# Optimization experiments

Hardware: AMD Instinct MI355X
Metric: run time of the kernel (lower is better)

The kernel has to match this reference:

```python
import jax, jax.numpy as jnp
import numpy as np

B, LI, LJ, D = 32, 512, 512, 512
NN_DIM = 256  # agg output dim = 2*NN_DIM = 512


def setup_inputs() -> dict:
    key = jax.random.key(0)
    k1, k2, k3 = jax.random.split(key, 3)
    i = jax.random.normal(k1, (B, LI, D), dtype=jnp.float32)
    j = jax.random.normal(k2, (B, LJ, D), dtype=jnp.float32)
    W_agg = jax.random.normal(k3, (D, 2 * NN_DIM), dtype=jnp.float32) * (1.0 / np.sqrt(D))
    b_agg = jnp.zeros((2 * NN_DIM,), dtype=jnp.float32)
    return {"i": i, "j": j, "W_agg": W_agg, "b_agg": b_agg}


def _agg(x, W, b):
    # shared aggregation net: Dense(2*nn_dim) + tanh, then mean-pool over time
    # x: [B, L, D] -> [B, 2*nn_dim]
    return jnp.mean(jnp.tanh(jnp.einsum('bld,dh->blh', x, W) + b), axis=1)


def reference(i, j, W_agg, b_agg):
    # cross-attention scores: [B, Li, Lj]
    weight = jnp.einsum('bik,bjk->bij', i, j)
    # row softmax (over Lj) -> weights to aggregate j per i-position
    weight_j = jax.nn.softmax(weight, axis=2)
    # column softmax (over Li) -> weights to aggregate i per j-position
    weight_i = jax.nn.softmax(weight, axis=1)
    weighted_i = jnp.einsum('bij,bid->bjd', weight_i, i)  # [B, Lj, D]
    weighted_j = jnp.einsum('bij,bjd->bid', weight_j, j)  # [B, Li, D]
    output_i = jnp.abs(i - weighted_j)  # [B, Li, D]
    output_j = jnp.abs(j - weighted_i)  # [B, Lj, D]
    oi = _agg(output_i, W_agg, b_agg)   # [B, 2*nn_dim]
    oj = _agg(output_j, W_agg, b_agg)   # [B, 2*nn_dim]
    # K.mean(K.stack([oi, oj], axis=1), axis=1)
    return 0.5 * (oi + oj)
```

## Files before the change

kernel.cpp:

```cpp
#include <hip/hip_runtime.h>
#include <math.h>

#define B_ 32
#define L_ 512
#define D_ 512
#define H_ 512

typedef unsigned short u16;
typedef _Float16 h16;
typedef h16 half8 __attribute__((ext_vector_type(8)));
typedef float f32x4 __attribute__((ext_vector_type(4)));

#define SW(r, c) ((c) ^ (((r) >> 1) & 3))

typedef __attribute__((address_space(1))) void gvoid;
typedef __attribute__((address_space(3))) void svoid;
__device__ __forceinline__ void async_cp16(const void* g, void* l) {
    __builtin_amdgcn_global_load_lds((gvoid*)g, (svoid*)l, 16, 0, 0);
}

__device__ __forceinline__ u16 f2h(float x) {
    h16 h = (h16)x;
    u16 r;
    __builtin_memcpy(&r, &h, 2);
    return r;
}
__device__ __forceinline__ float h2f(u16 u) {
    h16 h;
    __builtin_memcpy(&h, &u, 2);
    return (float)h;
}

__global__ __launch_bounds__(256) void cvt_all(const float* __restrict__ I,
                                               const float* __restrict__ Jm,
                                               const float* __restrict__ W,
                                               u16* __restrict__ Ih, u16* __restrict__ IhT,
                                               u16* __restrict__ Jh, u16* __restrict__ JhT,
                                               u16* __restrict__ WT,
                                               float* __restrict__ out) {
    const int z = blockIdx.z;
    const float* src;
    u16* h;
    u16* hT;
    size_t base;
    if (z < 32) {
        src = I; h = Ih; hT = IhT; base = (size_t)z * 512 * 512;
    } else if (z < 64) {
        src = Jm; h = Jh; hT = JhT; base = (size_t)(z - 32) * 512 * 512;
    } else {
        src = W; h = nullptr; hT = WT; base = 0;
        out[(blockIdx.y * 8 + blockIdx.x) * 256 + threadIdx.x] = 0.0f;
    }
    const int r0 = blockIdx.y * 64, c0 = blockIdx.x * 64;
    __shared__ u16 t[64][66];
    const int tid = threadIdx.x;
    const int tr = tid >> 4, tc4 = (tid & 15) * 4;
#pragma unroll
    for (int rep = 0; rep < 4; ++rep) {
        int r = rep * 16 + tr;
        f32x4 v = *(const f32x4*)(src + base + (size_t)(r0 + r) * 512 + c0 + tc4);
        unsigned h0 = f2h(v[0]), h1 = f2h(v[1]), h2 = f2h(v[2]), h3 = f2h(v[3]);
        if (h)
            *(uint2*)(h + base + (size_t)(r0 + r) * 512 + c0 + tc4) =
                make_uint2(h0 | (h1 << 16), h2 | (h3 << 16));
        t[r][tc4] = (u16)h0; t[r][tc4 + 1] = (u16)h1;
        t[r][tc4 + 2] = (u16)h2; t[r][tc4 + 3] = (u16)h3;
    }
    __syncthreads();
#pragma unroll
    for (int rep = 0; rep < 4; ++rep) {
        int r = rep * 16 + tr;
        unsigned a = t[tc4][r], b = t[tc4 + 1][r], c = t[tc4 + 2][r], d = t[tc4 + 3][r];
        *(uint2*)(hT + base + (size_t)(c0 + r) * 512 + r0 + tc4) =
            make_uint2(a | (b << 16), c | (d << 16));
    }
}

__global__ __launch_bounds__(256, 2) void score_mfma(const u16* __restrict__ Ih,
                                                     const u16* __restrict__ Jh,
                                                     float* __restrict__ S,
                                                     float* __restrict__ St) {
    const int b = blockIdx.z, i0 = blockIdx.y * 128, j0 = blockIdx.x * 128;
    __shared__ u16 Ah[128 * 32], Bh[128 * 32];
    const int tid = threadIdx.x;
    const int wave = tid >> 6, lane = tid & 63;
    const int wm = (wave >> 1) * 64, wn = (wave & 1) * 64;
    const int lr = lane & 15, q = lane >> 4;
    const size_t boff = (size_t)b * L_ * D_;
    const u16* Ibh = Ih + boff;
    const u16* Jbh = Jh + boff;

    f32x4 acc[4][4] = {};

    for (int k0 = 0; k0 < D_; k0 += 32) {
#pragma unroll
        for (int h = 0; h < 2; ++h) {
            int g = wave * 2 + h;
            int r = g * 16 + (lane >> 2);
            int cg = SW(r, lane & 3);
            async_cp16(Ibh + (size_t)(i0 + r) * D_ + k0 + cg * 8, (char*)Ah + g * 1024);
            async_cp16(Jbh + (size_t)(j0 + r) * D_ + k0 + cg * 8, (char*)Bh + g * 1024);
        }
        __syncthreads();
        half8 af[4], bf[4];
#pragma unroll
        for (int mi = 0; mi < 4; ++mi) {
            int r = wm + mi * 16 + lr;
            af[mi] = *(const half8*)&Ah[r * 32 + SW(r, q) * 8];
        }
#pragma unroll
        for (int ni = 0; ni < 4; ++ni) {
            int r = wn + ni * 16 + lr;
            bf[ni] = *(const half8*)&Bh[r * 32 + SW(r, q) * 8];
        }
#pragma unroll
        for (int mi = 0; mi < 4; ++mi)
#pragma unroll
            for (int ni = 0; ni < 4; ++ni)
                acc[mi][ni] = __builtin_amdgcn_mfma_f32_16x16x32_f16(af[mi], bf[ni], acc[mi][ni], 0, 0, 0);
        __syncthreads();
    }

    float* Sb = S + (size_t)b * L_ * L_;
    float* Stb = St + (size_t)b * L_ * L_;
#pragma unroll
    for (int mi = 0; mi < 4; ++mi)
#pragma unroll
        for (int ni = 0; ni < 4; ++ni) {
            int i = i0 + wm + mi * 16 + q * 4;
            int j = j0 + wn + ni * 16 + lr;
#pragma unroll
            for (int r4 = 0; r4 < 4; ++r4)
                Sb[(size_t)(i + r4) * L_ + j] = acc[mi][ni][r4];
            *(f32x4*)&Stb[(size_t)j * L_ + i] = acc[mi][ni];
        }
}

__global__ __launch_bounds__(256) void softmax_rows(const float* __restrict__ S,
                                                    u16* __restrict__ P) {
    const int row = blockIdx.x * 4 + (threadIdx.x >> 6);
    const int lane = threadIdx.x & 63;
    const float* Sr = S + (size_t)row * L_;
    f32x4 a = *(const f32x4*)(Sr + lane * 8);
    f32x4 b = *(const f32x4*)(Sr + lane * 8 + 4);
    float m = fmaxf(fmaxf(fmaxf(a[0], a[1]), fmaxf(a[2], a[3])),
                    fmaxf(fmaxf(b[0], b[1]), fmaxf(b[2], b[3])));
#pragma unroll
    for (int off = 32; off > 0; off >>= 1) m = fmaxf(m, __shfl_xor(m, off));
    float e[8];
    e[0] = __expf(a[0] - m); e[1] = __expf(a[1] - m);
    e[2] = __expf(a[2] - m); e[3] = __expf(a[3] - m);
    e[4] = __expf(b[0] - m); e[5] = __expf(b[1] - m);
    e[6] = __expf(b[2] - m); e[7] = __expf(b[3] - m);
    float s = ((e[0] + e[1]) + (e[2] + e[3])) + ((e[4] + e[5]) + (e[6] + e[7]));
#pragma unroll
    for (int off = 32; off > 0; off >>= 1) s += __shfl_xor(s, off);
    const float inv = 1.0f / s;
    uint4 o;
    o.x = (unsigned)f2h(e[0] * inv) | ((unsigned)f2h(e[1] * inv) << 16);
    o.y = (unsigned)f2h(e[2] * inv) | ((unsigned)f2h(e[3] * inv) << 16);
    o.z = (unsigned)f2h(e[4] * inv) | ((unsigned)f2h(e[5] * inv) << 16);
    o.w = (unsigned)f2h(e[6] * inv) | ((unsigned)f2h(e[7] * inv) << 16);
    *(uint4*)(P + (size_t)row * L_ + lane * 8) = o;
}

__global__ __launch_bounds__(256, 2) void absdiff_gemm(const u16* __restrict__ Prow,
                                                       const u16* __restrict__ Pcol,
                                                       const u16* __restrict__ JhT,
                                                       const u16* __restrict__ IhT,
                                                       const u16* __restrict__ Ih,
                                                       const u16* __restrict__ Jh,
                                                       u16* __restrict__ Xall) {
    const int z = blockIdx.z;
    const int side = z >> 5, b = z & 31;
    const u16* P = side ? Pcol : Prow;
    const u16* Vt = side ? IhT : JhT;
    const u16* Oh = side ? Jh : Ih;
    u16* Xout = Xall + (size_t)side * B_ * L_ * D_;
    const int i0 = blockIdx.x * 128, d0 = blockIdx.y * 128;
    __shared__ u16 As[128 * 32], Bs[128 * 32];
    const int tid = threadIdx.x;
    const int wave = tid >> 6, lane = tid & 63;
    const int wm = (wave >> 1) * 64, wn = (wave & 1) * 64;
    const int lr = lane & 15, q = lane >> 4;
    const u16* Pb = P + (size_t)b * L_ * L_;
    const u16* Vtb = Vt + (size_t)b * D_ * L_;

    f32x4 acc[4][4] = {};

    for (int k0 = 0; k0 < L_; k0 += 32) {
#pragma unroll
        for (int h = 0; h < 2; ++h) {
            int g = wave * 2 + h;
            int r = g * 16 + (lane >> 2);
            int cg = SW(r, lane & 3);
            async_cp16(Pb + (size_t)(i0 + r) * L_ + k0 + cg * 8, (char*)As + g * 1024);
            async_cp16(Vtb + (size_t)(d0 + r) * L_ + k0 + cg * 8, (char*)Bs + g * 1024);
        }
        __syncthreads();
        half8 af[4], bf[4];
#pragma unroll
        for (int mi = 0; mi < 4; ++mi) {
            int r = wm + mi * 16 + lr;
            af[mi] = *(const half8*)&As[r * 32 + SW(r, q) * 8];
        }
#pragma unroll
        for (int ni = 0; ni < 4; ++ni) {
            int r = wn + ni * 16 + lr;
            bf[ni] = *(const half8*)&Bs[r * 32 + SW(r, q) * 8];
        }
#pragma unroll
        for (int mi = 0; mi < 4; ++mi)
#pragma unroll
            for (int ni = 0; ni < 4; ++ni)
                acc[mi][ni] = __builtin_amdgcn_mfma_f32_16x16x32_f16(af[mi], bf[ni], acc[mi][ni], 0, 0, 0);
        __syncthreads();
    }

    const u16* Ob = Oh + (size_t)b * L_ * D_;
    u16* Xb = Xout + (size_t)b * L_ * D_;
#pragma unroll
    for (int mi = 0; mi < 4; ++mi)
#pragma unroll
        for (int ni = 0; ni < 4; ++ni) {
            int i = i0 + wm + mi * 16 + q * 4;
            int d = d0 + wn + ni * 16 + lr;
#pragma unroll
            for (int r4 = 0; r4 < 4; ++r4) {
                float x = fabsf(h2f(Ob[(size_t)(i + r4) * D_ + d]) - acc[mi][ni][r4]);
                Xb[(size_t)(i + r4) * D_ + d] = f2h(x);
            }
        }
}

__global__ __launch_bounds__(256, 2) void agg_mfma(const u16* __restrict__ Xall,
                                                   const u16* __restrict__ Wt,
                                                   const float* __restrict__ bias,
                                                   float* __restrict__ out) {
    const int z = blockIdx.z;
    const int bb = z & 31;
    const u16* Xb = Xall + (size_t)z * L_ * D_;
    const int l0 = blockIdx.x * 128, h0 = blockIdx.y * 128;
    __shared__ u16 As[128 * 32], Bs[128 * 32];
    const int tid = threadIdx.x;
    const int wave = tid >> 6, lane = tid & 63;
    const int wm = (wave >> 1) * 64, wn = (wave & 1) * 64;
    const int lr = lane & 15, q = lane >> 4;

    f32x4 acc[4][4] = {};

    for (int k0 = 0; k0 < D_; k0 += 32) {
#pragma unroll
        for (int h = 0; h < 2; ++h) {
            int g = wave * 2 + h;
            int r = g * 16 + (lane >> 2);
            int cg = SW(r, lane & 3);
            async_cp16(Xb + (size_t)(l0 + r) * D_ + k0 + cg * 8, (char*)As + g * 1024);
            async_cp16(Wt + (size_t)(h0 + r) * D_ + k0 + cg * 8, (char*)Bs + g * 1024);
        }
        __syncthreads();
        half8 af[4], bf[4];
#pragma unroll
        for (int mi = 0; mi < 4; ++mi) {
            int r = wm + mi * 16 + lr;
            af[mi] = *(const half8*)&As[r * 32 + SW(r, q) * 8];
        }
#pragma unroll
        for (int ni = 0; ni < 4; ++ni) {
            int r = wn + ni * 16 + lr;
            bf[ni] = *(const half8*)&Bs[r * 32 + SW(r, q) * 8];
        }
#pragma unroll
        for (int mi = 0; mi < 4; ++mi)
#pragma unroll
            for (int ni = 0; ni < 4; ++ni)
                acc[mi][ni] = __builtin_amdgcn_mfma_f32_16x16x32_f16(af[mi], bf[ni], acc[mi][ni], 0, 0, 0);
        __syncthreads();
    }

#pragma unroll
    for (int ni = 0; ni < 4; ++ni) {
        int hcol = h0 + wn + ni * 16 + lr;
        float bsv = bias[hcol];
        float ssum = 0.f;
#pragma unroll
        for (int mi = 0; mi < 4; ++mi)
#pragma unroll
            for (int r4 = 0; r4 < 4; ++r4)
                ssum += tanhf(acc[mi][ni][r4] + bsv);
        ssum += __shfl_xor(ssum, 16);
        ssum += __shfl_xor(ssum, 32);
        if (q == 0) atomicAdd(&out[bb * H_ + hcol], ssum * (0.5f / (float)L_));
    }
}

extern "C" void kernel_launch(void* const* d_in, const int* in_sizes, int n_in,
                              void* d_out, int out_size, void* d_ws, size_t ws_size,
                              hipStream_t stream) {
    const float* I = (const float*)d_in[0];
    const float* Jm = (const float*)d_in[1];
    const float* W = (const float*)d_in[2];
    const float* bias = (const float*)d_in[3];
    float* out = (float*)d_out;

    const size_t BLD = (size_t)B_ * L_ * D_;
    const size_t BLL = (size_t)B_ * L_ * L_;

    char* p = (char*)d_ws;
    auto give = [&](size_t bytes) {
        char* r = p;
        p += (bytes + 255) & ~(size_t)255;
        return r;
    };
    u16* Ih = (u16*)give(BLD * 2);
    u16* Jh = (u16*)give(BLD * 2);
    u16* IhT = (u16*)give(BLD * 2);
    u16* JhT = (u16*)give(BLD * 2);
    u16* WT = (u16*)give((size_t)D_ * H_ * 2);
    float* S = (float*)give(2 * BLL * 4);
    float* St = S + BLL;
    u16* Pblk = (u16*)give(2 * BLL * 2);
    u16* Prow = Pblk;
    u16* Pcol = Pblk + BLL;
    u16* Xall = (u16*)S;

    cvt_all<<<dim3(8, 8, 65), 256, 0, stream>>>(I, Jm, W, Ih, IhT, Jh, JhT, WT, out);
    score_mfma<<<dim3(4, 4, B_), 256, 0, stream>>>(Ih, Jh, S, St);
    softmax_rows<<<2 * B_ * L_ / 4, 256, 0, stream>>>(S, Prow);
    absdiff_gemm<<<dim3(4, 4, 2 * B_), 256, 0, stream>>>(Prow, Pcol, JhT, IhT, Ih, Jh, Xall);
    agg_mfma<<<dim3(4, 4, 2 * B_), 256, 0, stream>>>(Xall, WT, bias, out);
}
```

Baseline: 232.8 us.

## Fuse softmax into absdiff GEMM and remap blocks for XCD locality

```diff
diff --git a/kernel.cpp b/kernel.cpp
--- a/kernel.cpp
+++ b/kernel.cpp
@@ -29,6 +29,13 @@
     h16 h;
     __builtin_memcpy(&h, &u, 2);
     return (float)h;
+}
+
+__device__ __forceinline__ void xcd_decode(int n, int zgroups, int& z, int& tile) {
+    int xcd = n & 7, w = n >> 3;
+    z = xcd + 8 * (w >> 4);
+    tile = w & 15;
+    (void)zgroups;
 }
 
 __global__ __launch_bounds__(256) void cvt_all(const float* __restrict__ I,
@@ -80,7 +87,9 @@
                                                      const u16* __restrict__ Jh,
                                                      float* __restrict__ S,
                                                      float* __restrict__ St) {
-    const int b = blockIdx.z, i0 = blockIdx.y * 128, j0 = blockIdx.x * 128;
+    int b, tile;
+    xcd_decode(blockIdx.x, 4, b, tile);
+    const int i0 = (tile >> 2) * 128, j0 = (tile & 3) * 128;
     __shared__ u16 Ah[128 * 32], Bh[128 * 32];
     const int tid = threadIdx.x;
     const int wave = tid >> 6, lane = tid & 63;
@@ -136,55 +145,57 @@
         }
 }
 
-__global__ __launch_bounds__(256) void softmax_rows(const float* __restrict__ S,
-                                                    u16* __restrict__ P) {
-    const int row = blockIdx.x * 4 + (threadIdx.x >> 6);
-    const int lane = threadIdx.x & 63;
-    const float* Sr = S + (size_t)row * L_;
-    f32x4 a = *(const f32x4*)(Sr + lane * 8);
-    f32x4 b = *(const f32x4*)(Sr + lane * 8 + 4);
-    float m = fmaxf(fmaxf(fmaxf(a[0], a[1]), fmaxf(a[2], a[3])),
-                    fmaxf(fmaxf(b[0], b[1]), fmaxf(b[2], b[3])));
-#pragma unroll
-    for (int off = 32; off > 0; off >>= 1) m = fmaxf(m, __shfl_xor(m, off));
-    float e[8];
-    e[0] = __expf(a[0] - m); e[1] = __expf(a[1] - m);
-    e[2] = __expf(a[2] - m); e[3] = __expf(a[3] - m);
-    e[4] = __expf(b[0] - m); e[5] = __expf(b[1] - m);
-    e[6] = __expf(b[2] - m); e[7] = __expf(b[3] - m);
-    float s = ((e[0] + e[1]) + (e[2] + e[3])) + ((e[4] + e[5]) + (e[6] + e[7]));
-#pragma unroll
-    for (int off = 32; off > 0; off >>= 1) s += __shfl_xor(s, off);
-    const float inv = 1.0f / s;
-    uint4 o;
-    o.x = (unsigned)f2h(e[0] * inv) | ((unsigned)f2h(e[1] * inv) << 16);
-    o.y = (unsigned)f2h(e[2] * inv) | ((unsigned)f2h(e[3] * inv) << 16);
-    o.z = (unsigned)f2h(e[4] * inv) | ((unsigned)f2h(e[5] * inv) << 16);
-    o.w = (unsigned)f2h(e[6] * inv) | ((unsigned)f2h(e[7] * inv) << 16);
-    *(uint4*)(P + (size_t)row * L_ + lane * 8) = o;
-}
-
-__global__ __launch_bounds__(256, 2) void absdiff_gemm(const u16* __restrict__ Prow,
-                                                       const u16* __restrict__ Pcol,
-                                                       const u16* __restrict__ JhT,
-                                                       const u16* __restrict__ IhT,
-                                                       const u16* __restrict__ Ih,
-                                                       const u16* __restrict__ Jh,
-                                                       u16* __restrict__ Xall) {
-    const int z = blockIdx.z;
-    const int side = z >> 5, b = z & 31;
-    const u16* P = side ? Pcol : Prow;
-    const u16* Vt = side ? IhT : JhT;
-    const u16* Oh = side ? Jh : Ih;
-    u16* Xout = Xall + (size_t)side * B_ * L_ * D_;
-    const int i0 = blockIdx.x * 128, d0 = blockIdx.y * 128;
-    __shared__ u16 As[128 * 32], Bs[128 * 32];
+__global__ __launch_bounds__(256, 2) void absdiff_fused(const float* __restrict__ Sall,
+                                                        const u16* __restrict__ JhT,
+                                                        const u16* __restrict__ IhT,
+                                                        const u16* __restrict__ Ih,
+                                                        const u16* __restrict__ Jh,
+                                                        u16* __restrict__ Xall) {
+    int zz, tile;
+    xcd_decode(blockIdx.x, 8, zz, tile);
+    const int side = zz >> 5, b = zz & 31;
+    const int i0 = (tile >> 2) * 128, d0 = (tile & 3) * 128;
+    const u16* Vt = (side ? IhT : JhT) + (size_t)b * D_ * L_;
+    const u16* Oh = (side ? Jh : Ih) + (size_t)b * L_ * D_;
+    u16* Xb = Xall + (size_t)zz * L_ * D_;
+    const float* Sb = Sall + (size_t)zz * L_ * L_;
+
+    __shared__ u16 At[128 * 32], Bs[128 * 32];
+    __shared__ float red[128][2];
+    __shared__ float rmx[128], rsm[128];
     const int tid = threadIdx.x;
     const int wave = tid >> 6, lane = tid & 63;
     const int wm = (wave >> 1) * 64, wn = (wave & 1) * 64;
     const int lr = lane & 15, q = lane >> 4;
-    const u16* Pb = P + (size_t)b * L_ * L_;
-    const u16* Vtb = Vt + (size_t)b * D_ * L_;
+
+    {
+        const int rr = tid >> 1, half = tid & 1;
+        const float* rp = Sb + (size_t)(i0 + rr) * L_ + half * 256;
+        float m = -1e30f;
+#pragma unroll
+        for (int c = 0; c < 64; ++c) {
+            f32x4 v = *(const f32x4*)(rp + c * 4);
+            m = fmaxf(m, fmaxf(fmaxf(v[0], v[1]), fmaxf(v[2], v[3])));
+        }
+        red[rr][half] = m;
+        __syncthreads();
+        const float mrow = fmaxf(red[rr][0], red[rr][1]);
+        __syncthreads();
+        float s = 0.f;
+#pragma unroll
+        for (int c = 0; c < 64; ++c) {
+            f32x4 v = *(const f32x4*)(rp + c * 4);
+            s += (__expf(v[0] - mrow) + __expf(v[1] - mrow)) +
+                 (__expf(v[2] - mrow) + __expf(v[3] - mrow));
+        }
+        red[rr][half] = s;
+        __syncthreads();
+        if (half == 0) {
+            rmx[rr] = mrow;
+            rsm[rr] = 1.0f / (red[rr][0] + red[rr][1]);
+        }
+        __syncthreads();
+    }
 
     f32x4 acc[4][4] = {};
 
@@ -194,15 +205,34 @@
             int g = wave * 2 + h;
             int r = g * 16 + (lane >> 2);
             int cg = SW(r, lane & 3);
-            async_cp16(Pb + (size_t)(i0 + r) * L_ + k0 + cg * 8, (char*)As + g * 1024);
-            async_cp16(Vtb + (size_t)(d0 + r) * L_ + k0 + cg * 8, (char*)Bs + g * 1024);
+            async_cp16(Vt + (size_t)(d0 + r) * L_ + k0 + cg * 8, (char*)Bs + g * 1024);
+        }
+#pragma unroll
+        for (int h = 0; h < 2; ++h) {
+            int ch = h * 256 + tid;
+            int r = ch >> 2, cs = ch & 3;
+            int cg = SW(r, cs);
+            const float* sp = Sb + (size_t)(i0 + r) * L_ + k0 + cg * 8;
+            f32x4 v0 = *(const f32x4*)sp;
+            f32x4 v1 = *(const f32x4*)(sp + 4);
+            const float m = rmx[r], inv = rsm[r];
+            half8 pk;
+            pk[0] = (h16)(__expf(v0[0] - m) * inv);
+            pk[1] = (h16)(__expf(v0[1] - m) * inv);
+            pk[2] = (h16)(__expf(v0[2] - m) * inv);
+            pk[3] = (h16)(__expf(v0[3] - m) * inv);
+            pk[4] = (h16)(__expf(v1[0] - m) * inv);
+            pk[5] = (h16)(__expf(v1[1] - m) * inv);
+            pk[6] = (h16)(__expf(v1[2] - m) * inv);
+            pk[7] = (h16)(__expf(v1[3] - m) * inv);
+            *(half8*)((char*)At + ch * 16) = pk;
         }
         __syncthreads();
         half8 af[4], bf[4];
 #pragma unroll
         for (int mi = 0; mi < 4; ++mi) {
             int r = wm + mi * 16 + lr;
-            af[mi] = *(const half8*)&As[r * 32 + SW(r, q) * 8];
+            af[mi] = *(const half8*)&At[r * 32 + SW(r, q) * 8];
         }
 #pragma unroll
         for (int ni = 0; ni < 4; ++ni) {
@@ -217,8 +247,6 @@
         __syncthreads();
     }
 
-    const u16* Ob = Oh + (size_t)b * L_ * D_;
-    u16* Xb = Xout + (size_t)b * L_ * D_;
 #pragma unroll
     for (int mi = 0; mi < 4; ++mi)
 #pragma unroll
@@ -227,7 +255,7 @@
             int d = d0 + wn + ni * 16 + lr;
 #pragma unroll
             for (int r4 = 0; r4 < 4; ++r4) {
-                float x = fabsf(h2f(Ob[(size_t)(i + r4) * D_ + d]) - acc[mi][ni][r4]);
+                float x = fabsf(h2f(Oh[(size_t)(i + r4) * D_ + d]) - acc[mi][ni][r4]);
                 Xb[(size_t)(i + r4) * D_ + d] = f2h(x);
             }
         }
@@ -237,10 +265,11 @@
                                                    const u16* __restrict__ Wt,
                                                    const float* __restrict__ bias,
                                                    float* __restrict__ out) {
-    const int z = blockIdx.z;
-    const int bb = z & 31;
-    const u16* Xb = Xall + (size_t)z * L_ * D_;
-    const int l0 = blockIdx.x * 128, h0 = blockIdx.y * 128;
+    int zz, tile;
+    xcd_decode(blockIdx.x, 8, zz, tile);
+    const int bb = zz & 31;
+    const u16* Xb = Xall + (size_t)zz * L_ * D_;
+    const int l0 = (tile >> 2) * 128, h0 = (tile & 3) * 128;
     __shared__ u16 As[128 * 32], Bs[128 * 32];
     const int tid = threadIdx.x;
     const int wave = tid >> 6, lane = tid & 63;
@@ -319,14 +348,10 @@
     u16* WT = (u16*)give((size_t)D_ * H_ * 2);
     float* S = (float*)give(2 * BLL * 4);
     float* St = S + BLL;
-    u16* Pblk = (u16*)give(2 * BLL * 2);
-    u16* Prow = Pblk;
-    u16* Pcol = Pblk + BLL;
-    u16* Xall = (u16*)S;
+    u16* Xall = (u16*)give(2 * BLD * 2);
 
     cvt_all<<<dim3(8, 8, 65), 256, 0, stream>>>(I, Jm, W, Ih, IhT, Jh, JhT, WT, out);
-    score_mfma<<<dim3(4, 4, B_), 256, 0, stream>>>(Ih, Jh, S, St);
-    softmax_rows<<<2 * B_ * L_ / 4, 256, 0, stream>>>(S, Prow);
-    absdiff_gemm<<<dim3(4, 4, 2 * B_), 256, 0, stream>>>(Prow, Pcol, JhT, IhT, Ih, Jh, Xall);
-    agg_mfma<<<dim3(4, 4, 2 * B_), 256, 0, stream>>>(Xall, WT, bias, out);
-}
+    score_mfma<<<512, 256, 0, stream>>>(Ih, Jh, S, St);
+    absdiff_fused<<<1024, 256, 0, stream>>>(S, JhT, IhT, Ih, Jh, Xall);
+    agg_mfma<<<1024, 256, 0, stream>>>(Xall, WT, bias, out);
+}
```

Measured after the change: 242.7 us. 1.04x slower.
